# Performance work log

Measured on AMD Instinct MI355X. Metric: run time of the kernel, lower is better.

The kernel has to match this reference:

```python
import jax, jax.numpy as jnp
import numpy as np

N = 80000
E = 1280000
C_IN, HID, C_OUT = 3, 64, 1
DEPTH = 3
KS = [40000, 20000, 10000]  # ceil(0.5 * n) per pooling level
EPS = 1e-5


def gcn_conv(x, W, src, dst, ew, n, fill=2.0):
    # PyG GCNConv with add_self_loops=True; improved => self-loop weight fill=2.0
    h = x @ W                                           # [n, F]
    deg = jax.ops.segment_sum(ew, dst, num_segments=n) + fill
    dinv = jax.lax.rsqrt(deg)
    norm = dinv[src] * ew * dinv[dst]                   # [E]
    agg = jax.ops.segment_sum(norm[:, None] * h[src], dst, num_segments=n)
    return agg + (fill * dinv * dinv)[:, None] * h      # self-loop term


def batchnorm(x, gamma, beta):
    # BatchNorm1d in training mode: biased batch stats over the node dim
    mu = jnp.mean(x, axis=0)
    var = jnp.var(x, axis=0)
    return gamma * (x - mu) * jax.lax.rsqrt(var + EPS) + beta


def gcn_block(x, src, dst, ew, n, W, gamma, beta, fill=2.0):
    return jax.nn.relu(batchnorm(gcn_conv(x, W, src, dst, ew, n, fill), gamma, beta))


def topk_pool(x, src, dst, ew, w, k):
    # TopKPooling with ReLU nonlinearity: score = relu(x.w / ||w||)
    n = x.shape[0]
    score = jax.nn.relu(x @ w / jnp.linalg.norm(w))
    sc, perm = jax.lax.top_k(score, k)
    xk = x[perm] * sc[:, None]
    # filter_adj with fixed edge count: invalid edges get weight 0 (no-op in GCN)
    mapping = jnp.full((n,), -1, dtype=src.dtype).at[perm].set(
        jnp.arange(k, dtype=src.dtype))
    ns, nd = mapping[src], mapping[dst]
    valid = (ns >= 0) & (nd >= 0)
    ns = jnp.where(valid, ns, 0)
    nd = jnp.where(valid, nd, 0)
    new_ew = jnp.where(valid, ew, jnp.zeros((), ew.dtype))
    return xk, ns, nd, new_ew, perm


def _forward(x, edge_index, Wd, gd, bd, pw, Wu, gu, bu, W_out):
    src, dst = edge_index[0], edge_index[1]
    ew = jnp.ones(src.shape, x.dtype)
    n = x.shape[0]
    x = gcn_block(x, src, dst, ew, n, Wd[0], gd[0], bd[0])
    xs, sds, ews, perms = [x], [(src, dst)], [ew], []
    for i in range(DEPTH):
        x, src, dst, ew, perm = topk_pool(x, src, dst, ew, pw[i], KS[i])
        x = gcn_block(x, src, dst, ew, KS[i], Wd[i + 1], gd[i + 1], bd[i + 1])
        if i < DEPTH - 1:
            xs.append(x); sds.append((src, dst)); ews.append(ew)
        perms.append(perm)
    for i in range(DEPTH):
        j = DEPTH - 1 - i
        res = xs[j]; src, dst = sds[j]; ew = ews[j]; perm = perms[j]
        up = jnp.zeros_like(res).at[perm].set(x)
        x = res + up
        if i < DEPTH - 1:
            x = gcn_block(x, src, dst, ew, res.shape[0], Wu[i], gu[i], bu[i])
        else:
            x = jax.nn.sigmoid(
                gcn_conv(x, W_out, src, dst, ew, res.shape[0], fill=1.0))
    return x


def setup_inputs() -> dict:
    key = jax.random.key(0)
    ks = jax.random.split(key, 16)
    nrm = lambda k, shape: jax.random.normal(k, shape, jnp.float32) * 0.1
    inp = {
        "x": jax.random.normal(ks[0], (N, C_IN), jnp.float32),
        "edge_index": jax.random.randint(ks[1], (2, E), 0, N, jnp.int32),
    }
    dims = [(C_IN, HID)] + [(HID, HID)] * DEPTH
    ki = 2
    for l, (a, b) in enumerate(dims):
        inp[f"W_d{l}"] = nrm(ks[ki], (a, b)); ki += 1
        inp[f"g_d{l}"] = jnp.ones((b,), jnp.float32)
        inp[f"b_d{l}"] = jnp.zeros((b,), jnp.float32)
    for l in range(DEPTH):
        inp[f"pw{l}"] = nrm(ks[ki], (HID,)); ki += 1
    for l in range(DEPTH - 1):
        inp[f"W_u{l}"] = nrm(ks[ki], (HID, HID)); ki += 1
        inp[f"g_u{l}"] = jnp.ones((HID,), jnp.float32)
        inp[f"b_u{l}"] = jnp.zeros((HID,), jnp.float32)
    inp["W_out"] = nrm(ks[ki], (HID, C_OUT))
    return inp


def reference(x, edge_index, W_d0, g_d0, b_d0, W_d1, g_d1, b_d1, W_d2, g_d2,
              b_d2, W_d3, g_d3, b_d3, pw0, pw1, pw2, W_u0, g_u0, b_u0,
              W_u1, g_u1, b_u1, W_out):
    Wd = [W_d0, W_d1, W_d2, W_d3]
    gd = [g_d0, g_d1, g_d2, g_d3]
    bd = [b_d0, b_d1, b_d2, b_d3]
    pw = [pw0, pw1, pw2]
    Wu = [W_u0, W_u1]
    gu = [g_u0, g_u1]
    bu = [b_u0, b_u1]
    return _forward(x, edge_index, Wd, gd, bd, pw, Wu, gu, bu, W_out)
```

## Files before the change

kernel.cpp:

```cpp
#include <hip/hip_runtime.h>
#include <cstdint>
#include <utility>

#define NN0 80000
#define NE 1280000
#define MMB_GRID 2048
#define EB 2048
#define ENB 625
#define E9B 512

static inline int cdiv(int a, int b){ return (a+b-1)/b; }

__global__ void k_conv64(const int* __restrict__ rp, const int* __restrict__ col,
                         const float* __restrict__ dinv, const float* __restrict__ x,
                         const float* __restrict__ W, float* __restrict__ out,
                         float* __restrict__ part, int n){
  __shared__ float yl[4][64];
  __shared__ float ls[64], lq[64];
  int lane = threadIdx.x & 63, w = threadIdx.x >> 6;
  if (threadIdx.x < 64){ ls[threadIdx.x] = 0.f; lq[threadIdx.x] = 0.f; }
  __syncthreads();
  float sa = 0.f, sq = 0.f;
  int wid = blockIdx.x*4 + w, nw = gridDim.x*4;
  for (int i = wid; i < n; i += nw){
    int beg = rp[i], end = rp[i+1];
    float di = dinv[i];
    float y = 0.f;
    int j = beg;
    for (; j + 4 <= end; j += 4){
      int s0 = col[j], s1 = col[j+1], s2 = col[j+2], s3 = col[j+3];
      float y0 = dinv[s0]*x[s0*64+lane];
      float y1 = dinv[s1]*x[s1*64+lane];
      float y2 = dinv[s2]*x[s2*64+lane];
      float y3 = dinv[s3]*x[s3*64+lane];
      y += (y0+y1) + (y2+y3);
    }
    for (; j < end; j++){ int s = col[j]; y += dinv[s]*x[s*64+lane]; }
    y = di*y + 2.f*di*di*x[i*64+lane];
    yl[w][lane] = y;
    float acc = 0.f;
    #pragma unroll
    for (int k2 = 0; k2 < 64; k2++)
      acc += yl[w][k2]*W[k2*64+lane];
    out[i*64+lane] = acc;
    sa += acc; sq += acc*acc;
  }
  atomicAdd(&ls[lane], sa); atomicAdd(&lq[lane], sq);
  __syncthreads();
  if (threadIdx.x < 128)
    part[blockIdx.x*128 + threadIdx.x] =
      (threadIdx.x < 64) ? ls[threadIdx.x] : lq[threadIdx.x-64];
}

__global__ void k_matmul_bn3(const float* __restrict__ x, const float* __restrict__ W,
                             float* __restrict__ h, float* __restrict__ part, int n){
  __shared__ float ls[64], lq[64];
  int f = threadIdx.x & 63;
  float sa = 0.f, sq = 0.f;
  int total = n*64, stride = gridDim.x*blockDim.x;
  for (int t = blockIdx.x*blockDim.x + threadIdx.x; t < total; t += stride){
    int i = t >> 6;
    float s = x[i*3]*W[f] + x[i*3+1]*W[64+f] + x[i*3+2]*W[128+f];
    h[t] = s; sa += s; sq += s*s;
  }
  if (threadIdx.x < 64){ ls[threadIdx.x] = 0.f; lq[threadIdx.x] = 0.f; }
  __syncthreads();
  atomicAdd(&ls[f], sa); atomicAdd(&lq[f], sq);
  __syncthreads();
  if (threadIdx.x < 128)
    part[blockIdx.x*128 + threadIdx.x] =
      (threadIdx.x < 64) ? ls[threadIdx.x] : lq[threadIdx.x-64];
}

__global__ void k_stats_reduce(const float* __restrict__ part, float* __restrict__ stats){
  int c = blockIdx.x, lane = threadIdx.x;
  float s = 0.f;
  for (int b = lane; b < MMB_GRID; b += 64) s += part[b*128 + c];
  for (int o = 32; o > 0; o >>= 1) s += __shfl_xor(s, o);
  if (lane == 0) stats[c] = s;
}

__global__ void k_matvec(const float* __restrict__ x, const float* __restrict__ W,
                         float* __restrict__ h1, int n){
  int lane = threadIdx.x & 63, w = threadIdx.x >> 6;
  int wid = blockIdx.x*4 + w, nw = gridDim.x*4;
  float wv = W[lane];
  for (int i = wid; i < n; i += nw){
    float v = x[i*64+lane]*wv;
    for (int o = 32; o > 0; o >>= 1) v += __shfl_xor(v, o);
    if (lane == 0) h1[i] = v;
  }
}

__global__ void k_ehist9(const int* __restrict__ key, int* __restrict__ hist, int shift){
  __shared__ int lh[E9B];
  for (int d = threadIdx.x; d < E9B; d += 256) lh[d] = 0;
  __syncthreads();
  int base = blockIdx.x*EB + threadIdx.x;
  #pragma unroll
  for (int u = 0; u < 8; u++)
    atomicAdd(&lh[(key[base + u*256] >> shift) & 511], 1);
  __syncthreads();
  for (int d = threadIdx.x; d < E9B; d += 256)
    hist[d*ENB + blockIdx.x] = lh[d];
}

__global__ void k_escatter9(const int* __restrict__ keyin, const int* __restrict__ valin,
                            int* __restrict__ keyout, int* __restrict__ valout,
                            const int* __restrict__ hist, int shift){
  __shared__ int dbase[E9B], run[E9B], wcnt[4][E9B];
  int t = threadIdx.x, lane = t & 63, w = t >> 6;
  for (int d = t; d < E9B; d += 256){ dbase[d] = hist[d*ENB + blockIdx.x]; run[d] = 0; }
  __syncthreads();
  for (int u = 0; u < 8; u++){
    for (int d = t; d < E9B; d += 256){ wcnt[0][d]=0; wcnt[1][d]=0; wcnt[2][d]=0; wcnt[3][d]=0; }
    __syncthreads();
    int g = blockIdx.x*EB + u*256 + t;
    int kk = keyin[g], vv = valin[g];
    int d = (kk >> shift) & 511;
    unsigned long long m = ~0ull;
    #pragma unroll
    for (int b = 0; b < 9; b++){
      unsigned long long bal = __ballot((d >> b) & 1);
      m &= ((d >> b) & 1) ? bal : ~bal;
    }
    int rnk = __popcll(m & ((1ull << lane) - 1ull));
    if (rnk == 0) wcnt[w][d] = __popcll(m);
    __syncthreads();
    int off2 = run[d] + rnk;
    for (int w2 = 0; w2 < w; w2++) off2 += wcnt[w2][d];
    int pos = dbase[d] + off2;
    keyout[pos] = kk; valout[pos] = vv;
    __syncthreads();
    for (int d2 = t; d2 < E9B; d2 += 256)
      run[d2] += wcnt[0][d2] + wcnt[1][d2] + wcnt[2][d2] + wcnt[3][d2];
    __syncthreads();
  }
}

__global__ void k_rp_search(const int* __restrict__ skey, int* __restrict__ rp,
                            float* __restrict__ dinvA, float* __restrict__ dinvB, int n){
  int i = blockIdx.x*blockDim.x + threadIdx.x;
  if (i >= n) return;
  int lo = 0, hi = NE;
  while (lo < hi){ int mid = (lo+hi)>>1; if (skey[mid] < i) lo = mid+1; else hi = mid; }
  int a = lo;
  lo = a; hi = NE;
  while (lo < hi){ int mid = (lo+hi)>>1; if (skey[mid] < i+1) lo = mid+1; else hi = mid; }
  int b2 = lo;
  rp[i] = a;
  if (i == n-1) rp[n] = NE;
  float deg = (float)(b2 - a);
  dinvA[i] = 1.0f/sqrtf(deg + 2.f);
  dinvB[i] = 1.0f/sqrtf(deg + 1.f);
}

__global__ void k_scan_part(const int* __restrict__ in, int* __restrict__ bsum, int n){
  __shared__ int ws[256];
  int base = blockIdx.x*2048 + threadIdx.x*8;
  int s = 0;
  #pragma unroll
  for (int u = 0; u < 8; u++){ int i = base+u; if (i < n) s += in[i]; }
  ws[threadIdx.x] = s; __syncthreads();
  for (int st = 128; st > 0; st >>= 1){
    if (threadIdx.x < st) ws[threadIdx.x] += ws[threadIdx.x+st];
    __syncthreads();
  }
  if (threadIdx.x == 0) bsum[blockIdx.x] = ws[0];
}

__global__ void k_scan_fin_rp(const int* __restrict__ in, const int* __restrict__ bsum, int nb,
                              int* __restrict__ rp, float* __restrict__ dinvA, int n){
  __shared__ int bws[256]; __shared__ int ws[256];
  int t = threadIdx.x;
  bws[t] = (t < nb) ? bsum[t] : 0; __syncthreads();
  for (int st = 1; st < 256; st <<= 1){
    int a = (t >= st) ? bws[t-st] : 0; __syncthreads();
    bws[t] += a; __syncthreads();
  }
  int blockoff = (blockIdx.x == 0) ? 0 : bws[blockIdx.x-1];
  int base = blockIdx.x*2048 + t*8;
  int v[8]; int s = 0;
  #pragma unroll
  for (int u = 0; u < 8; u++){ int i = base+u; v[u] = (i < n) ? in[i] : 0; s += v[u]; }
  ws[t] = s; __syncthreads();
  for (int st = 1; st < 256; st <<= 1){
    int a = (t >= st) ? ws[t-st] : 0; __syncthreads();
    ws[t] += a; __syncthreads();
  }
  int off = blockoff + ws[t] - s;
  #pragma unroll
  for (int u = 0; u < 8; u++){
    int i = base+u;
    if (i < n){
      rp[i] = off; off += v[u];
      dinvA[i] = 1.0f/sqrtf((float)v[u] + 2.f);
      if (i == n-1) rp[n] = off;
    }
  }
}

__global__ void k_scan_fin_flat(int* __restrict__ data, const int* __restrict__ bsum, int nb, int n){
  __shared__ int bws[256]; __shared__ int ws[256];
  int t = threadIdx.x;
  bws[t] = (t < nb) ? bsum[t] : 0; __syncthreads();
  for (int st = 1; st < 256; st <<= 1){
    int a = (t >= st) ? bws[t-st] : 0; __syncthreads();
    bws[t] += a; __syncthreads();
  }
  int blockoff = (blockIdx.x == 0) ? 0 : bws[blockIdx.x-1];
  int base = blockIdx.x*2048 + t*8;
  int v[8]; int s = 0;
  #pragma unroll
  for (int u = 0; u < 8; u++){ int i = base+u; v[u] = (i < n) ? data[i] : 0; s += v[u]; }
  ws[t] = s; __syncthreads();
  for (int st = 1; st < 256; st <<= 1){
    int a = (t >= st) ? ws[t-st] : 0; __syncthreads();
    ws[t] += a; __syncthreads();
  }
  int off = blockoff + ws[t] - s;
  #pragma unroll
  for (int u = 0; u < 8; u++){
    int i = base+u;
    if (i < n){ data[i] = off; off += v[u]; }
  }
}

__global__ void k_hist_mapped(const int* __restrict__ rp_p, const int* __restrict__ col_p,
                              const int* __restrict__ mapv, int* __restrict__ indeg, int np){
  int d = blockIdx.x*blockDim.x + threadIdx.x;
  if (d >= np) return;
  int md = mapv[d];
  if (md < 0) return;
  int c = 0, e = rp_p[d+1];
  int j = rp_p[d];
  for (; j + 4 <= e; j += 4){
    int c0 = (mapv[col_p[j]]   >= 0);
    int c1 = (mapv[col_p[j+1]] >= 0);
    int c2 = (mapv[col_p[j+2]] >= 0);
    int c3 = (mapv[col_p[j+3]] >= 0);
    c += (c0+c1) + (c2+c3);
  }
  for (; j < e; j++) if (mapv[col_p[j]] >= 0) c++;
  indeg[md] = c;
}
__global__ void k_scatter_mapped(const int* __restrict__ rp_p, const int* __restrict__ col_p,
                                 const int* __restrict__ mapv, const int* __restrict__ rp_c,
                                 int* __restrict__ col_c, int np){
  int d = blockIdx.x*blockDim.x + threadIdx.x;
  if (d >= np) return;
  int md = mapv[d];
  if (md < 0) return;
  int pos = rp_c[md], e = rp_p[d+1];
  int j = rp_p[d];
  for (; j + 4 <= e; j += 4){
    int m0 = mapv[col_p[j]], m1 = mapv[col_p[j+1]];
    int m2 = mapv[col_p[j+2]], m3 = mapv[col_p[j+3]];
    if (m0 >= 0) col_c[pos++] = m0;
    if (m1 >= 0) col_c[pos++] = m1;
    if (m2 >= 0) col_c[pos++] = m2;
    if (m3 >= 0) col_c[pos++] = m3;
  }
  for (; j < e; j++){
    int ms = mapv[col_p[j]];
    if (ms >= 0) col_c[pos++] = ms;
  }
}

__global__ void k_gather3(const int* __restrict__ rp, const int* __restrict__ col,
                          const float* __restrict__ dinv, const float* __restrict__ x,
                          float* __restrict__ y, int n){
  int i = blockIdx.x*blockDim.x + threadIdx.x;
  if (i >= n) return;
  int beg = rp[i], end = rp[i+1];
  float di = dinv[i];
  float a0 = 0.f, a1 = 0.f, a2 = 0.f;
  int j = beg;
  for (; j + 4 <= end; j += 4){
    int s0 = col[j], s1 = col[j+1], s2 = col[j+2], s3 = col[j+3];
    float d0 = dinv[s0], d1 = dinv[s1], d2 = dinv[s2], d3 = dinv[s3];
    a0 += d0*x[s0*3+0] + d1*x[s1*3+0] + d2*x[s2*3+0] + d3*x[s3*3+0];
    a1 += d0*x[s0*3+1] + d1*x[s1*3+1] + d2*x[s2*3+1] + d3*x[s3*3+1];
    a2 += d0*x[s0*3+2] + d1*x[s1*3+2] + d2*x[s2*3+2] + d3*x[s3*3+2];
  }
  for (; j < end; j++){
    int s = col[j];
    float ds = dinv[s];
    a0 += ds*x[s*3+0]; a1 += ds*x[s*3+1]; a2 += ds*x[s*3+2];
  }
  float sl = 2.f*di*di;
  y[i*3+0] = di*a0 + sl*x[i*3+0];
  y[i*3+1] = di*a1 + sl*x[i*3+1];
  y[i*3+2] = di*a2 + sl*x[i*3+2];
}

__global__ void k_gather_sig(const int* __restrict__ rp, const int* __restrict__ col,
                             const float* __restrict__ dinv, const float* __restrict__ h1,
                             float* __restrict__ out, int n){
  int i = blockIdx.x*blockDim.x + threadIdx.x;
  if (i >= n) return;
  int beg = rp[i], end = rp[i+1];
  float di = dinv[i];
  float acc = 0.f;
  int j = beg;
  for (; j + 4 <= end; j += 4){
    int s0 = col[j], s1 = col[j+1], s2 = col[j+2], s3 = col[j+3];
    float v0 = dinv[s0]*h1[s0];
    float v1 = dinv[s1]*h1[s1];
    float v2 = dinv[s2]*h1[s2];
    float v3 = dinv[s3]*h1[s3];
    acc += (v0+v1) + (v2+v3);
  }
  for (; j < end; j++) acc += dinv[col[j]]*h1[col[j]];
  float v = di*acc + di*di*h1[i];
  out[i] = 1.f/(1.f+expf(-v));
}

__global__ void k_bnrelu(float* __restrict__ x, const float* __restrict__ stats,
                         const float* __restrict__ gamma, const float* __restrict__ beta,
                         int n) {
  int t = blockIdx.x*blockDim.x + threadIdx.x;
  if (t >= n*64) return;
  int f = t & 63;
  float inv_n = 1.0f/(float)n;
  float mu = stats[f]*inv_n;
  float var = stats[64+f]*inv_n - mu*mu;
  float v = gamma[f]*(x[t]-mu)*(1.0f/sqrtf(var+1e-5f)) + beta[f];
  x[t] = fmaxf(v, 0.f);
}

__global__ void k_bnrelu_score(float* __restrict__ x, const float* __restrict__ stats,
                               const float* __restrict__ gamma, const float* __restrict__ beta,
                               const float* __restrict__ pw,
                               float* __restrict__ score, unsigned* __restrict__ key,
                               int* __restrict__ idx, int n, int P){
  int lane = threadIdx.x & 63, w = threadIdx.x >> 6;
  int wid = blockIdx.x*4 + w, nw = gridDim.x*4;
  float inv_n = 1.f/(float)n;
  float mu = stats[lane]*inv_n;
  float var = stats[64+lane]*inv_n - mu*mu;
  float gs = gamma[lane]*(1.f/sqrtf(var+1e-5f));
  float bt = beta[lane];
  float pv = pw[lane];
  float q = pv*pv;
  for (int o = 32; o > 0; o >>= 1) q += __shfl_xor(q, o);
  float qn = 1.f/sqrtf(q);
  for (int i = wid; i < n; i += nw){
    float v = fmaxf(gs*(x[i*64+lane]-mu)+bt, 0.f);
    x[i*64+lane] = v;
    float s = v*pv;
    for (int o = 32; o > 0; o >>= 1) s += __shfl_xor(s, o);
    if (lane == 0){
      float sc = fmaxf(s*qn, 0.f);
      score[i] = sc; key[i] = ~__float_as_uint(sc); idx[i] = i;
    }
  }
  for (int g = n + wid; g < P; g += nw)
    if (lane == 0){ key[g] = 0xFFFFFFFFu; idx[g] = 0; }
}

__global__ void k_radix_hist(const unsigned* __restrict__ key, int* __restrict__ hist,
                             int shift, int nblk){
  __shared__ int lh[256];
  lh[threadIdx.x] = 0; __syncthreads();
  int base = blockIdx.x*1024 + threadIdx.x;
  #pragma unroll
  for (int u = 0; u < 4; u++){
    unsigned d = (key[base + u*256] >> shift) & 255u;
    atomicAdd(&lh[d], 1);
  }
  __syncthreads();
  hist[threadIdx.x*nblk + blockIdx.x] = lh[threadIdx.x];
}

__global__ void k_radix_scatter(const unsigned* __restrict__ keyin, const int* __restrict__ idxin,
                                unsigned* __restrict__ keyout, int* __restrict__ idxout,
                                const int* __restrict__ hist, int shift, int nblk){
  __shared__ int dbase[256], run[256], sc[256];
  __shared__ int wcnt[4][256];
  int t = threadIdx.x, lane = t & 63, w = t >> 6;
  int pre = 0, tot = 0;
  for (int b = 0; b < nblk; b++){
    int v = hist[t*nblk + b];
    if (b < blockIdx.x) pre += v;
    tot += v;
  }
  sc[t] = tot; __syncthreads();
  for (int st = 1; st < 256; st <<= 1){
    int a = (t >= st) ? sc[t-st] : 0; __syncthreads();
    sc[t] += a; __syncthreads();
  }
  dbase[t] = sc[t] - tot + pre;
  run[t] = 0;
  for (int u = 0; u < 4; u++){
    wcnt[0][t] = 0; wcnt[1][t] = 0; wcnt[2][t] = 0; wcnt[3][t] = 0;
    __syncthreads();
    int g = blockIdx.x*1024 + u*256 + t;
    unsigned kk = keyin[g]; int id = idxin[g];
    unsigned d = (kk >> shift) & 255u;
    unsigned long long m = ~0ull;
    #pragma unroll
    for (int b = 0; b < 8; b++){
      unsigned long long bal = __ballot((d >> b) & 1u);
      m &= ((d >> b) & 1u) ? bal : ~bal;
    }
    int rnk = __popcll(m & ((1ull << lane) - 1ull));
    if (rnk == 0) wcnt[w][d] = __popcll(m);
    __syncthreads();
    int off2 = run[d] + rnk;
    for (int w2 = 0; w2 < w; w2++) off2 += wcnt[w2][d];
    int pos = dbase[d] + off2;
    keyout[pos] = kk; idxout[pos] = id;
    __syncthreads();
    run[t] += wcnt[0][t] + wcnt[1][t] + wcnt[2][t] + wcnt[3][t];
    __syncthreads();
  }
}

__global__ void k_select_gather(const int* __restrict__ idxs, const float* __restrict__ x,
                                const float* __restrict__ score, int* __restrict__ perm,
                                int* __restrict__ mapv, float* __restrict__ xk, int n, int k){
  int t = blockIdx.x*blockDim.x + threadIdx.x;
  if (t < n){
    int i = idxs[t];
    mapv[i] = (t < k) ? t : -1;
    if (t < k) perm[t] = i;
  }
  if (t < k*64){
    int r = t >> 6, f = t & 63;
    int i = idxs[r];
    xk[t] = x[i*64+f]*score[i];
  }
}

__global__ void k_scatter_add(const float* __restrict__ xup, const int* __restrict__ perm,
                              float* __restrict__ res, int k) {
  int t = blockIdx.x*blockDim.x + threadIdx.x;
  if (t >= k*64) return;
  int r = t >> 6, f = t & 63;
  res[perm[r]*64+f] += xup[t];
}

extern "C" void kernel_launch(void* const* d_in, const int* in_sizes, int n_in,
                              void* d_out, int out_size, void* d_ws, size_t ws_size,
                              hipStream_t stream) {
  const float* x_in = (const float*)d_in[0];
  const int* ei = (const int*)d_in[1];
  const int* src0 = ei;
  const int* dst0 = ei + NE;
  const float* W_d[4] = {(const float*)d_in[2],(const float*)d_in[5],(const float*)d_in[8],(const float*)d_in[11]};
  const float* g_d[4] = {(const float*)d_in[3],(const float*)d_in[6],(const float*)d_in[9],(const float*)d_in[12]};
  const float* b_d[4] = {(const float*)d_in[4],(const float*)d_in[7],(const float*)d_in[10],(const float*)d_in[13]};
  const float* pw[3]  = {(const float*)d_in[14],(const float*)d_in[15],(const float*)d_in[16]};
  const float* W_u[2] = {(const float*)d_in[17],(const float*)d_in[20]};
  const float* g_u[2] = {(const float*)d_in[18],(const float*)d_in[21]};
  const float* b_u[2] = {(const float*)d_in[19],(const float*)d_in[22]};
  const float* W_out  = (const float*)d_in[23];
  float* out = (float*)d_out;

  float* base = (float*)d_ws;
  size_t off = 0;
  auto alloc = [&](size_t nf){ float* p = base + off; off += nf; return p; };
  float* x0 = alloc(5120000);
  float* x1 = alloc(2560000);
  float* x2 = alloc(1280000);
  float* x3 = alloc(640000);
  float* A  = alloc(2560000);
  float* h3 = alloc(240000);
  int* col0 = (int*)alloc(NE);
  int* col1 = (int*)alloc(NE);
  int* col2 = (int*)alloc(NE);
  int* col3 = (int*)alloc(NE);
  int* ek1 = (int*)alloc(NE);
  int* ev1 = (int*)alloc(NE);
  int* ek2 = (int*)alloc(NE);
  int* rp0 = (int*)alloc(80001);
  int* rp1 = (int*)alloc(40001);
  int* rp2 = (int*)alloc(20001);
  int* rp3 = (int*)alloc(10001);
  int* indeg  = (int*)alloc(NN0);
  float* dinv0  = alloc(NN0);
  float* dinv0f = alloc(NN0);
  float* dinv1  = alloc(40000);
  float* dinv2  = alloc(20000);
  float* dinv3  = alloc(10000);
  float* score = alloc(NN0);
  int* mapv = (int*)alloc(NN0);
  int* p0 = (int*)alloc(40000);
  int* p1 = (int*)alloc(20000);
  int* p2 = (int*)alloc(10000);
  float* stats = alloc(128);
  float* part  = alloc(MMB_GRID*128);
  unsigned* keyA = (unsigned*)alloc(81920);
  unsigned* keyB = (unsigned*)alloc(81920);
  int* idxA = (int*)alloc(81920);
  int* idxB = (int*)alloc(81920);
  int* hist = (int*)alloc(81920);
  int* ehist = (int*)alloc(E9B*ENB);
  int* bsum = (int*)alloc(256);
  (void)ws_size; (void)in_sizes; (void)n_in; (void)out_size;

  const int B = 256;

  auto scan_flat = [&](int* data, int n2){
    int nb = cdiv(n2, 2048);
    k_scan_part    <<<nb, 256, 0, stream>>>(data, bsum, n2);
    k_scan_fin_flat<<<nb, 256, 0, stream>>>(data, bsum, nb, n2);
  };
  auto scan_csr = [&](const int* indeg_, int* rp, float* dv, int n2){
    int nb = cdiv(n2, 2048);
    k_scan_part  <<<nb, 256, 0, stream>>>(indeg_, bsum, n2);
    k_scan_fin_rp<<<nb, 256, 0, stream>>>(indeg_, bsum, nb, rp, dv, n2);
  };

  auto conv = [&](const float* xin, const float* W, int n,
                  const int* rp, const int* col, const float* dv, float* dstb){
    k_conv64<<<MMB_GRID, B, 0, stream>>>(rp, col, dv, xin, W, dstb, part, n);
    k_stats_reduce<<<128, 64, 0, stream>>>(part, stats);
  };

  auto pool = [&](float* xb, const float* g, const float* bt, const float* w,
                  int n, int k, int* pm, float* xk){
    int nblk = cdiv(n, 1024), P = nblk*1024;
    k_bnrelu_score<<<1024, B, 0, stream>>>(xb, stats, g, bt, w, score, keyA, idxA, n, P);
    unsigned* ka = keyA; int* ia = idxA; unsigned* kb = keyB; int* ib = idxB;
    for (int pass = 0; pass < 4; pass++){
      k_radix_hist   <<<nblk, 256, 0, stream>>>(ka, hist, pass*8, nblk);
      k_radix_scatter<<<nblk, 256, 0, stream>>>(ka, ia, kb, ib, hist, pass*8, nblk);
      std::swap(ka, kb); std::swap(ia, ib);
    }
    k_select_gather<<<cdiv(k*64,B), B, 0, stream>>>(ia, xb, score, pm, mapv, xk, n, k);
  };

  auto csr_mapped = [&](const int* rp_p, const int* col_p, int np, int nc,
                        int* rp_c, int* col_c, float* dv){
    k_hist_mapped<<<cdiv(np,B), B, 0, stream>>>(rp_p, col_p, mapv, indeg, np);
    scan_csr(indeg, rp_c, dv, nc);
    k_scatter_mapped<<<cdiv(np,B), B, 0, stream>>>(rp_p, col_p, mapv, rp_c, col_c, np);
  };

  k_ehist9   <<<ENB, B, 0, stream>>>(dst0, ehist, 0);
  scan_flat(ehist, E9B*ENB);
  k_escatter9<<<ENB, B, 0, stream>>>(dst0, src0, ek1, ev1, ehist, 0);
  k_ehist9   <<<ENB, B, 0, stream>>>(ek1, ehist, 9);
  scan_flat(ehist, E9B*ENB);
  k_escatter9<<<ENB, B, 0, stream>>>(ek1, ev1, ek2, col0, ehist, 9);
  k_rp_search<<<cdiv(NN0,B), B, 0, stream>>>(ek2, rp0, dinv0, dinv0f, NN0);

  k_gather3   <<<cdiv(NN0,B), B, 0, stream>>>(rp0, col0, dinv0, x_in, h3, NN0);
  k_matmul_bn3<<<MMB_GRID, B, 0, stream>>>(h3, W_d[0], x0, part, NN0);
  k_stats_reduce<<<128, 64, 0, stream>>>(part, stats);
  pool(x0, g_d[0], b_d[0], pw[0], NN0, 40000, p0, A);
  csr_mapped(rp0, col0, NN0, 40000, rp1, col1, dinv1);

  conv(A, W_d[1], 40000, rp1, col1, dinv1, x1);
  pool(x1, g_d[1], b_d[1], pw[1], 40000, 20000, p1, A);
  csr_mapped(rp1, col1, 40000, 20000, rp2, col2, dinv2);

  conv(A, W_d[2], 20000, rp2, col2, dinv2, x2);
  pool(x2, g_d[2], b_d[2], pw[2], 20000, 10000, p2, A);
  csr_mapped(rp2, col2, 20000, 10000, rp3, col3, dinv3);

  conv(A, W_d[3], 10000, rp3, col3, dinv3, x3);
  k_bnrelu<<<cdiv(10000*64,B), B, 0, stream>>>(x3, stats, g_d[3], b_d[3], 10000);

  k_scatter_add<<<cdiv(10000*64,B), B, 0, stream>>>(x3, p2, x2, 10000);
  conv(x2, W_u[0], 20000, rp2, col2, dinv2, A);
  k_bnrelu<<<cdiv(20000*64,B), B, 0, stream>>>(A, stats, g_u[0], b_u[0], 20000);

  k_scatter_add<<<cdiv(20000*64,B), B, 0, stream>>>(A, p1, x1, 20000);
  conv(x1, W_u[1], 40000, rp1, col1, dinv1, A);
  k_bnrelu<<<cdiv(40000*64,B), B, 0, stream>>>(A, stats, g_u[1], b_u[1], 40000);

  k_scatter_add<<<cdiv(40000*64,B), B, 0, stream>>>(A, p0, x0, 40000);

  float* h1 = score;
  k_matvec<<<512, B, 0, stream>>>(x0, W_out, h1, NN0);
  k_gather_sig<<<cdiv(NN0,B), B, 0, stream>>>(rp0, col0, dinv0f, h1, out, NN0);
}
```

Baseline: 758.7 us.

## Fuse top-k pooling into persistent kernel with grid barriers; use 6-bit edge radix

```diff
diff --git a/kernel.cpp b/kernel.cpp
--- a/kernel.cpp
+++ b/kernel.cpp
@@ -7,7 +7,7 @@
 #define MMB_GRID 2048
 #define EB 2048
 #define ENB 625
-#define E9B 512
+#define SG 256
 
 static inline int cdiv(int a, int b){ return (a+b-1)/b; }
 
@@ -92,35 +92,39 @@
   }
 }
 
-__global__ void k_ehist9(const int* __restrict__ key, int* __restrict__ hist, int shift){
-  __shared__ int lh[E9B];
-  for (int d = threadIdx.x; d < E9B; d += 256) lh[d] = 0;
+__global__ void k_zero_i(int* __restrict__ p, int n){
+  int t = blockIdx.x*blockDim.x + threadIdx.x;
+  if (t < n) p[t] = 0;
+}
+
+__global__ void k_ehist6(const int* __restrict__ key, int* __restrict__ hist, int shift){
+  __shared__ int lh[64];
+  if (threadIdx.x < 64) lh[threadIdx.x] = 0;
   __syncthreads();
   int base = blockIdx.x*EB + threadIdx.x;
   #pragma unroll
   for (int u = 0; u < 8; u++)
-    atomicAdd(&lh[(key[base + u*256] >> shift) & 511], 1);
-  __syncthreads();
-  for (int d = threadIdx.x; d < E9B; d += 256)
-    hist[d*ENB + blockIdx.x] = lh[d];
-}
-
-__global__ void k_escatter9(const int* __restrict__ keyin, const int* __restrict__ valin,
+    atomicAdd(&lh[(key[base + u*256] >> shift) & 63], 1);
+  __syncthreads();
+  if (threadIdx.x < 64) hist[threadIdx.x*ENB + blockIdx.x] = lh[threadIdx.x];
+}
+
+__global__ void k_escatter6(const int* __restrict__ keyin, const int* __restrict__ valin,
                             int* __restrict__ keyout, int* __restrict__ valout,
                             const int* __restrict__ hist, int shift){
-  __shared__ int dbase[E9B], run[E9B], wcnt[4][E9B];
+  __shared__ int dbase[64], run[64], wcnt[4][64];
   int t = threadIdx.x, lane = t & 63, w = t >> 6;
-  for (int d = t; d < E9B; d += 256){ dbase[d] = hist[d*ENB + blockIdx.x]; run[d] = 0; }
+  if (t < 64){ dbase[t] = hist[t*ENB + blockIdx.x]; run[t] = 0; }
   __syncthreads();
   for (int u = 0; u < 8; u++){
-    for (int d = t; d < E9B; d += 256){ wcnt[0][d]=0; wcnt[1][d]=0; wcnt[2][d]=0; wcnt[3][d]=0; }
+    if (t < 64){ wcnt[0][t]=0; wcnt[1][t]=0; wcnt[2][t]=0; wcnt[3][t]=0; }
     __syncthreads();
     int g = blockIdx.x*EB + u*256 + t;
     int kk = keyin[g], vv = valin[g];
-    int d = (kk >> shift) & 511;
+    int d = (kk >> shift) & 63;
     unsigned long long m = ~0ull;
     #pragma unroll
-    for (int b = 0; b < 9; b++){
+    for (int b = 0; b < 6; b++){
       unsigned long long bal = __ballot((d >> b) & 1);
       m &= ((d >> b) & 1) ? bal : ~bal;
     }
@@ -132,8 +136,7 @@
     int pos = dbase[d] + off2;
     keyout[pos] = kk; valout[pos] = vv;
     __syncthreads();
-    for (int d2 = t; d2 < E9B; d2 += 256)
-      run[d2] += wcnt[0][d2] + wcnt[1][d2] + wcnt[2][d2] + wcnt[3][d2];
+    if (t < 64) run[t] += wcnt[0][t] + wcnt[1][t] + wcnt[2][t] + wcnt[3][t];
     __syncthreads();
   }
 }
@@ -329,107 +332,153 @@
   x[t] = fmaxf(v, 0.f);
 }
 
-__global__ void k_bnrelu_score(float* __restrict__ x, const float* __restrict__ stats,
-                               const float* __restrict__ gamma, const float* __restrict__ beta,
-                               const float* __restrict__ pw,
-                               float* __restrict__ score, unsigned* __restrict__ key,
-                               int* __restrict__ idx, int n, int P){
-  int lane = threadIdx.x & 63, w = threadIdx.x >> 6;
-  int wid = blockIdx.x*4 + w, nw = gridDim.x*4;
-  float inv_n = 1.f/(float)n;
-  float mu = stats[lane]*inv_n;
-  float var = stats[64+lane]*inv_n - mu*mu;
-  float gs = gamma[lane]*(1.f/sqrtf(var+1e-5f));
-  float bt = beta[lane];
-  float pv = pw[lane];
-  float q = pv*pv;
-  for (int o = 32; o > 0; o >>= 1) q += __shfl_xor(q, o);
-  float qn = 1.f/sqrtf(q);
-  for (int i = wid; i < n; i += nw){
-    float v = fmaxf(gs*(x[i*64+lane]-mu)+bt, 0.f);
-    x[i*64+lane] = v;
-    float s = v*pv;
-    for (int o = 32; o > 0; o >>= 1) s += __shfl_xor(s, o);
-    if (lane == 0){
-      float sc = fmaxf(s*qn, 0.f);
-      score[i] = sc; key[i] = ~__float_as_uint(sc); idx[i] = i;
-    }
-  }
-  for (int g = n + wid; g < P; g += nw)
-    if (lane == 0){ key[g] = 0xFFFFFFFFu; idx[g] = 0; }
-}
-
-__global__ void k_radix_hist(const unsigned* __restrict__ key, int* __restrict__ hist,
-                             int shift, int nblk){
+__device__ __forceinline__ void gbar(int* cnt, int gen){
+  __syncthreads();
+  if (threadIdx.x == 0){
+    __threadfence();
+    atomicAdd(cnt, 1);
+    int target = SG*gen;
+    while (atomicAdd(cnt, 0) < target) ;
+    __threadfence();
+  }
+  __syncthreads();
+}
+
+__global__ __launch_bounds__(256, 1)
+void k_pool(float* __restrict__ x, const float* __restrict__ part,
+            float* __restrict__ stats,
+            const float* __restrict__ gamma, const float* __restrict__ beta,
+            const float* __restrict__ pw, float* __restrict__ score,
+            unsigned* __restrict__ keyA, int* __restrict__ idxA,
+            unsigned* __restrict__ keyB, int* __restrict__ idxB,
+            int* __restrict__ hist, int* __restrict__ rowsum,
+            int* __restrict__ perm, int* __restrict__ mapv,
+            float* __restrict__ xk, int* __restrict__ cnt, int n, int k){
   __shared__ int lh[256];
-  lh[threadIdx.x] = 0; __syncthreads();
-  int base = blockIdx.x*1024 + threadIdx.x;
-  #pragma unroll
-  for (int u = 0; u < 4; u++){
-    unsigned d = (key[base + u*256] >> shift) & 255u;
-    atomicAdd(&lh[d], 1);
-  }
-  __syncthreads();
-  hist[threadIdx.x*nblk + blockIdx.x] = lh[threadIdx.x];
-}
-
-__global__ void k_radix_scatter(const unsigned* __restrict__ keyin, const int* __restrict__ idxin,
-                                unsigned* __restrict__ keyout, int* __restrict__ idxout,
-                                const int* __restrict__ hist, int shift, int nblk){
-  __shared__ int dbase[256], run[256], sc[256];
-  __shared__ int wcnt[4][256];
-  int t = threadIdx.x, lane = t & 63, w = t >> 6;
-  int pre = 0, tot = 0;
-  for (int b = 0; b < nblk; b++){
-    int v = hist[t*nblk + b];
-    if (b < blockIdx.x) pre += v;
-    tot += v;
-  }
-  sc[t] = tot; __syncthreads();
-  for (int st = 1; st < 256; st <<= 1){
-    int a = (t >= st) ? sc[t-st] : 0; __syncthreads();
-    sc[t] += a; __syncthreads();
-  }
-  dbase[t] = sc[t] - tot + pre;
-  run[t] = 0;
-  for (int u = 0; u < 4; u++){
-    wcnt[0][t] = 0; wcnt[1][t] = 0; wcnt[2][t] = 0; wcnt[3][t] = 0;
-    __syncthreads();
-    int g = blockIdx.x*1024 + u*256 + t;
-    unsigned kk = keyin[g]; int id = idxin[g];
-    unsigned d = (kk >> shift) & 255u;
-    unsigned long long m = ~0ull;
-    #pragma unroll
-    for (int b = 0; b < 8; b++){
-      unsigned long long bal = __ballot((d >> b) & 1u);
-      m &= ((d >> b) & 1u) ? bal : ~bal;
-    }
-    int rnk = __popcll(m & ((1ull << lane) - 1ull));
-    if (rnk == 0) wcnt[w][d] = __popcll(m);
-    __syncthreads();
-    int off2 = run[d] + rnk;
-    for (int w2 = 0; w2 < w; w2++) off2 += wcnt[w2][d];
-    int pos = dbase[d] + off2;
-    keyout[pos] = kk; idxout[pos] = id;
-    __syncthreads();
-    run[t] += wcnt[0][t] + wcnt[1][t] + wcnt[2][t] + wcnt[3][t];
-    __syncthreads();
-  }
-}
-
-__global__ void k_select_gather(const int* __restrict__ idxs, const float* __restrict__ x,
-                                const float* __restrict__ score, int* __restrict__ perm,
-                                int* __restrict__ mapv, float* __restrict__ xk, int n, int k){
-  int t = blockIdx.x*blockDim.x + threadIdx.x;
-  if (t < n){
-    int i = idxs[t];
-    mapv[i] = (t < k) ? t : -1;
-    if (t < k) perm[t] = i;
-  }
-  if (t < k*64){
-    int r = t >> 6, f = t & 63;
-    int i = idxs[r];
-    xk[t] = x[i*64+f]*score[i];
+  __shared__ int srow[128];
+  __shared__ int db[256], run[256], wcnt[4][256], rb[256], sc[256];
+  __shared__ float red[256];
+  int t = threadIdx.x, b = blockIdx.x;
+  int lane = t & 63, w = t >> 6;
+  int nblk = (n + 1023)/1024, P = nblk*1024;
+  int gen = 0;
+
+  if (b < 128){
+    float s = 0.f;
+    for (int u = t; u < MMB_GRID; u += 256) s += part[u*128 + b];
+    red[t] = s; __syncthreads();
+    for (int st2 = 128; st2 > 0; st2 >>= 1){
+      if (t < st2) red[t] += red[t+st2];
+      __syncthreads();
+    }
+    if (t == 0) stats[b] = red[0];
+  }
+  gbar(cnt, ++gen);
+
+  {
+    float inv_n = 1.f/(float)n;
+    float mu = stats[lane]*inv_n;
+    float var = stats[64+lane]*inv_n - mu*mu;
+    float gs = gamma[lane]*(1.f/sqrtf(var+1e-5f));
+    float bt = beta[lane];
+    float pv = pw[lane];
+    float q = pv*pv;
+    for (int o = 32; o > 0; o >>= 1) q += __shfl_xor(q, o);
+    float qn = 1.f/sqrtf(q);
+    int wid = b*4 + w, nw = SG*4;
+    for (int i = wid; i < n; i += nw){
+      float v = fmaxf(gs*(x[i*64+lane]-mu)+bt, 0.f);
+      x[i*64+lane] = v;
+      float s = v*pv;
+      for (int o = 32; o > 0; o >>= 1) s += __shfl_xor(s, o);
+      if (lane == 0){
+        float scv = fmaxf(s*qn, 0.f);
+        score[i] = scv; keyA[i] = ~__float_as_uint(scv); idxA[i] = i;
+      }
+    }
+    for (int g = n + wid; g < P; g += nw)
+      if (lane == 0){ keyA[g] = 0xFFFFFFFFu; idxA[g] = 0; }
+  }
+  gbar(cnt, ++gen);
+
+  unsigned* ka = keyA; int* ia = idxA; unsigned* kb = keyB; int* ib = idxB;
+  for (int pass = 0; pass < 4; pass++){
+    int shift = pass*8;
+    for (int c = b; c < nblk; c += SG){
+      lh[t] = 0; __syncthreads();
+      int base = c*1024 + t;
+      #pragma unroll
+      for (int u = 0; u < 4; u++)
+        atomicAdd(&lh[(ka[base + u*256] >> shift) & 255u], 1);
+      __syncthreads();
+      hist[t*nblk + c] = lh[t];
+      __syncthreads();
+    }
+    gbar(cnt, ++gen);
+    {
+      int d = b;
+      if (t < nblk) srow[t] = hist[d*nblk + t];
+      __syncthreads();
+      if (t == 0){
+        int acc = 0;
+        for (int c = 0; c < nblk; c++){ int v = srow[c]; srow[c] = acc; acc += v; }
+        rowsum[d] = acc;
+      }
+      __syncthreads();
+      if (t < nblk) hist[d*nblk + t] = srow[t];
+    }
+    gbar(cnt, ++gen);
+    {
+      int v = rowsum[t];
+      sc[t] = v; __syncthreads();
+      for (int st2 = 1; st2 < 256; st2 <<= 1){
+        int a = (t >= st2) ? sc[t-st2] : 0; __syncthreads();
+        sc[t] += a; __syncthreads();
+      }
+      rb[t] = sc[t] - v;
+      __syncthreads();
+      for (int c = b; c < nblk; c += SG){
+        db[t] = rb[t] + hist[t*nblk + c];
+        run[t] = 0;
+        __syncthreads();
+        for (int u = 0; u < 4; u++){
+          wcnt[0][t] = 0; wcnt[1][t] = 0; wcnt[2][t] = 0; wcnt[3][t] = 0;
+          __syncthreads();
+          int g = c*1024 + u*256 + t;
+          unsigned kk = ka[g]; int id = ia[g];
+          unsigned d = (kk >> shift) & 255u;
+          unsigned long long m = ~0ull;
+          #pragma unroll
+          for (int bb = 0; bb < 8; bb++){
+            unsigned long long bal = __ballot((d >> bb) & 1u);
+            m &= ((d >> bb) & 1u) ? bal : ~bal;
+          }
+          int rnk = __popcll(m & ((1ull << lane) - 1ull));
+          if (rnk == 0) wcnt[w][d] = __popcll(m);
+          __syncthreads();
+          int off2 = run[d] + rnk;
+          for (int w2 = 0; w2 < w; w2++) off2 += wcnt[w2][d];
+          int pos = db[d] + off2;
+          kb[pos] = kk; ib[pos] = id;
+          __syncthreads();
+          run[t] += wcnt[0][t] + wcnt[1][t] + wcnt[2][t] + wcnt[3][t];
+          __syncthreads();
+        }
+      }
+    }
+    gbar(cnt, ++gen);
+    { unsigned* tmp = ka; ka = kb; kb = tmp; }
+    { int* tmp = ia; ia = ib; ib = tmp; }
+  }
+  for (int t2 = b*256 + t; t2 < k*64; t2 += SG*256){
+    if (t2 < n){
+      int i = ia[t2];
+      mapv[i] = (t2 < k) ? t2 : -1;
+      if (t2 < k) perm[t2] = i;
+    }
+    int r = t2 >> 6, f = t2 & 63;
+    int i = ia[r];
+    xk[t2] = x[i*64+f]*score[i];
   }
 }
 
@@ -474,6 +523,7 @@
   int* ek1 = (int*)alloc(NE);
   int* ev1 = (int*)alloc(NE);
   int* ek2 = (int*)alloc(NE);
+  int* ev2 = (int*)alloc(NE);
   int* rp0 = (int*)alloc(80001);
   int* rp1 = (int*)alloc(40001);
   int* rp2 = (int*)alloc(20001);
@@ -496,8 +546,10 @@
   int* idxA = (int*)alloc(81920);
   int* idxB = (int*)alloc(81920);
   int* hist = (int*)alloc(81920);
-  int* ehist = (int*)alloc(E9B*ENB);
+  int* rowsum = (int*)alloc(256);
+  int* ehist = (int*)alloc(64*ENB);
   int* bsum = (int*)alloc(256);
+  int* pcnt = (int*)alloc(8);
   (void)ws_size; (void)in_sizes; (void)n_in; (void)out_size;
 
   const int B = 256;
@@ -516,20 +568,13 @@
   auto conv = [&](const float* xin, const float* W, int n,
                   const int* rp, const int* col, const float* dv, float* dstb){
     k_conv64<<<MMB_GRID, B, 0, stream>>>(rp, col, dv, xin, W, dstb, part, n);
-    k_stats_reduce<<<128, 64, 0, stream>>>(part, stats);
   };
 
   auto pool = [&](float* xb, const float* g, const float* bt, const float* w,
-                  int n, int k, int* pm, float* xk){
-    int nblk = cdiv(n, 1024), P = nblk*1024;
-    k_bnrelu_score<<<1024, B, 0, stream>>>(xb, stats, g, bt, w, score, keyA, idxA, n, P);
-    unsigned* ka = keyA; int* ia = idxA; unsigned* kb = keyB; int* ib = idxB;
-    for (int pass = 0; pass < 4; pass++){
-      k_radix_hist   <<<nblk, 256, 0, stream>>>(ka, hist, pass*8, nblk);
-      k_radix_scatter<<<nblk, 256, 0, stream>>>(ka, ia, kb, ib, hist, pass*8, nblk);
-      std::swap(ka, kb); std::swap(ia, ib);
-    }
-    k_select_gather<<<cdiv(k*64,B), B, 0, stream>>>(ia, xb, score, pm, mapv, xk, n, k);
+                  int n, int k, int* pm, float* xk, int* cnt){
+    k_pool<<<SG, 256, 0, stream>>>(xb, part, stats, g, bt, w, score,
+                                   keyA, idxA, keyB, idxB, hist, rowsum,
+                                   pm, mapv, xk, cnt, n, k);
   };
 
   auto csr_mapped = [&](const int* rp_p, const int* col_p, int np, int nc,
@@ -539,37 +584,44 @@
     k_scatter_mapped<<<cdiv(np,B), B, 0, stream>>>(rp_p, col_p, mapv, rp_c, col_c, np);
   };
 
-  k_ehist9   <<<ENB, B, 0, stream>>>(dst0, ehist, 0);
-  scan_flat(ehist, E9B*ENB);
-  k_escatter9<<<ENB, B, 0, stream>>>(dst0, src0, ek1, ev1, ehist, 0);
-  k_ehist9   <<<ENB, B, 0, stream>>>(ek1, ehist, 9);
-  scan_flat(ehist, E9B*ENB);
-  k_escatter9<<<ENB, B, 0, stream>>>(ek1, ev1, ek2, col0, ehist, 9);
-  k_rp_search<<<cdiv(NN0,B), B, 0, stream>>>(ek2, rp0, dinv0, dinv0f, NN0);
+  k_zero_i<<<1, 64, 0, stream>>>(pcnt, 8);
+
+  k_ehist6   <<<ENB, B, 0, stream>>>(dst0, ehist, 0);
+  scan_flat(ehist, 64*ENB);
+  k_escatter6<<<ENB, B, 0, stream>>>(dst0, src0, ek1, ev1, ehist, 0);
+  k_ehist6   <<<ENB, B, 0, stream>>>(ek1, ehist, 6);
+  scan_flat(ehist, 64*ENB);
+  k_escatter6<<<ENB, B, 0, stream>>>(ek1, ev1, ek2, ev2, ehist, 6);
+  k_ehist6   <<<ENB, B, 0, stream>>>(ek2, ehist, 12);
+  scan_flat(ehist, 64*ENB);
+  k_escatter6<<<ENB, B, 0, stream>>>(ek2, ev2, ek1, col0, ehist, 12);
+  k_rp_search<<<cdiv(NN0,B), B, 0, stream>>>(ek1, rp0, dinv0, dinv0f, NN0);
 
   k_gather3   <<<cdiv(NN0,B), B, 0, stream>>>(rp0, col0, dinv0, x_in, h3, NN0);
   k_matmul_bn3<<<MMB_GRID, B, 0, stream>>>(h3, W_d[0], x0, part, NN0);
+  pool(x0, g_d[0], b_d[0], pw[0], NN0, 40000, p0, A, &pcnt[0]);
+  csr_mapped(rp0, col0, NN0, 40000, rp1, col1, dinv1);
+
+  conv(A, W_d[1], 40000, rp1, col1, dinv1, x1);
+  pool(x1, g_d[1], b_d[1], pw[1], 40000, 20000, p1, A, &pcnt[1]);
+  csr_mapped(rp1, col1, 40000, 20000, rp2, col2, dinv2);
+
+  conv(A, W_d[2], 20000, rp2, col2, dinv2, x2);
+  pool(x2, g_d[2], b_d[2], pw[2], 20000, 10000, p2, A, &pcnt[2]);
+  csr_mapped(rp2, col2, 20000, 10000, rp3, col3, dinv3);
+
+  conv(A, W_d[3], 10000, rp3, col3, dinv3, x3);
   k_stats_reduce<<<128, 64, 0, stream>>>(part, stats);
-  pool(x0, g_d[0], b_d[0], pw[0], NN0, 40000, p0, A);
-  csr_mapped(rp0, col0, NN0, 40000, rp1, col1, dinv1);
-
-  conv(A, W_d[1], 40000, rp1, col1, dinv1, x1);
-  pool(x1, g_d[1], b_d[1], pw[1], 40000, 20000, p1, A);
-  csr_mapped(rp1, col1, 40000, 20000, rp2, col2, dinv2);
-
-  conv(A, W_d[2], 20000, rp2, col2, dinv2, x2);
-  pool(x2, g_d[2], b_d[2], pw[2], 20000, 10000, p2, A);
-  csr_mapped(rp2, col2, 20000, 10000, rp3, col3, dinv3);
-
-  conv(A, W_d[3], 10000, rp3, col3, dinv3, x3);
   k_bnrelu<<<cdiv(10000*64,B), B, 0, stream>>>(x3, stats, g_d[3], b_d[3], 10000);
 
   k_scatter_add<<<cdiv(10000*64,B), B, 0, stream>>>(x3, p2, x2, 10000);
   conv(x2, W_u[0], 20000, rp2, col2, dinv2, A);
+  k_stats_reduce<<<128, 64, 0, stream>>>(part, stats);
   k_bnrelu<<<cdiv(20000*64,B), B, 0, stream>>>(A, stats, g_u[0], b_u[0], 20000);
 
   k_scatter_add<<<cdiv(20000*64,B), B, 0, stream>>>(A, p1, x1, 20000);
   conv(x1, W_u[1], 40000, rp1, col1, dinv1, A);
+  k_stats_reduce<<<128, 64, 0, stream>>>(part, stats);
   k_bnrelu<<<cdiv(40000*64,B), B, 0, stream>>>(A, stats, g_u[1], b_u[1], 40000);
 
   k_scatter_add<<<cdiv(40000*64,B), B, 0, stream>>>(A, p0, x0, 40000);
```

Result: slower. 1.405 ms (+85.1%).
